# Kernel optimization log

Hardware: AMD Instinct MI355X
Metric: run time of the kernel (lower is better)

## Reference

```python
import jax, jax.numpy as jnp
import numpy as np

N_NODES = 50000
N_EDGES = 600000
IN_DIM = 128
OUT_DIM = 128
N_REL = 32
N_BASES = 4
BN_EPS = 1e-5


def setup_inputs() -> dict:
    key = jax.random.key(0)
    ks = jax.random.split(key, 8)
    entity_emb = jax.random.normal(ks[0], (N_NODES, IN_DIM), dtype=jnp.float32)
    bases = jax.random.normal(ks[1], (N_BASES, IN_DIM, OUT_DIM), dtype=jnp.float32) * 0.05
    coefficients = jax.random.normal(ks[2], (N_REL, N_BASES), dtype=jnp.float32) * 0.5
    W_loop = jax.random.normal(ks[3], (IN_DIM, OUT_DIM), dtype=jnp.float32) * 0.05
    b_loop = jnp.zeros((OUT_DIM,), dtype=jnp.float32)
    gamma = jnp.ones((OUT_DIM,), dtype=jnp.float32)
    beta = jnp.zeros((OUT_DIM,), dtype=jnp.float32)
    edge_index = jax.random.randint(ks[4], (2, N_EDGES), 0, N_NODES, dtype=jnp.int32)
    edge_type = jax.random.randint(ks[5], (N_EDGES,), 0, N_REL, dtype=jnp.int32)
    return {"entity_emb": entity_emb, "bases": bases, "coefficients": coefficients,
            "W_loop": W_loop, "b_loop": b_loop, "gamma": gamma, "beta": beta,
            "edge_index": edge_index, "edge_type": edge_type}


def reference(entity_emb, bases, coefficients, W_loop, b_loop, gamma, beta, edge_index, edge_type):
    N = entity_emb.shape[0]
    # self-loop linear
    out = entity_emb @ W_loop + b_loop  # [N, out_dim]
    # basis decomposition: per-relation weight W[r] = sum_b coeff[r,b] * bases[b]
    W = jnp.einsum('rb,bio->rio', coefficients, bases)  # [R, in, out]
    src, dst = edge_index[0], edge_index[1]
    # per-edge message: entity_emb[src_e] @ W[edge_type_e]  (vectorizes the per-relation loop)
    msg = jnp.einsum('ei,eio->eo', entity_emb[src], W[edge_type])  # [E, out]
    out = out + jax.ops.segment_sum(msg, dst, num_segments=N)
    # degree normalization (in-degree over all edges, clamped at 1)
    deg = jax.ops.segment_sum(jnp.ones_like(dst, dtype=out.dtype), dst, num_segments=N)
    out = out / jnp.maximum(deg, 1.0)[:, None]
    # BatchNorm1d (training mode: biased batch stats over node dim)
    mean = jnp.mean(out, axis=0)
    var = jnp.mean((out - mean) ** 2, axis=0)
    out = (out - mean) / jnp.sqrt(var + BN_EPS) * gamma + beta
    return jax.nn.relu(out)
```

## Files before the change

kernel.cpp:

```cpp
#include <hip/hip_runtime.h>
#include <cstdint>

#define NN 50000
#define NE 600000

typedef unsigned short ushort_t;
typedef __bf16 bf16_t;
typedef __attribute__((ext_vector_type(8))) bf16_t bf16x8;
typedef __attribute__((ext_vector_type(8))) ushort_t ushort8;
typedef __attribute__((ext_vector_type(4))) float f32x4;

#define G_OFF    0ul
#define XBF_OFF  12800000ul
#define CNT_OFF  16000000ul
#define CUR_OFF  16050000ul
#define BSUM_OFF 16100000ul
#define BSCN_OFF 16100128ul
#define CS_OFF   16100256ul
#define CSQ_OFF  16100384ul
#define WT_OFF   16100512ul

__device__ __forceinline__ float2 bf2_to_f2(uint32_t u) {
    float2 r;
    r.x = __uint_as_float(u << 16);
    r.y = __uint_as_float(u & 0xffff0000u);
    return r;
}

__device__ __forceinline__ ushort_t f2bf(float f) {
    uint32_t u = __float_as_uint(f);
    u = (u + 0x7fffu + ((u >> 16) & 1u)) >> 16;
    return (ushort_t)u;
}

__device__ __forceinline__ uint32_t f2bf2(float x, float y) {
    return (uint32_t)f2bf(x) | ((uint32_t)f2bf(y) << 16);
}

__device__ __forceinline__ int swz(int g, int r) {
    return (g & 0x78) | ((g ^ r) & 7);
}

__global__ __launch_bounds__(256) void k_prep(
    const float* __restrict__ Wl, const float* __restrict__ bases,
    ushort_t* __restrict__ WT)
{
    const int i = blockIdx.x * 256 + threadIdx.x;
    if (i >= 128 * 640) return;
    const int n = i / 640;
    const int kk = i - n * 640;
    float v;
    if (kk < 128) v = Wl[kk * 128 + n];
    else {
        const int j = kk - 128;
        v = bases[(size_t)(j >> 7) * 16384 + (j & 127) * 128 + n];
    }
    WT[i] = f2bf(v);
}

__global__ __launch_bounds__(256) void k_cast(
    const float* __restrict__ X, ushort_t* __restrict__ Xbf)
{
    const int i = blockIdx.x * 256 + threadIdx.x;
    if (i >= NN * 16) return;
    const float4* p = (const float4*)(X + (size_t)i * 8);
    const float4 a = p[0], b = p[1];
    ushort_t t8[8] = { f2bf(a.x), f2bf(a.y), f2bf(a.z), f2bf(a.w),
                       f2bf(b.x), f2bf(b.y), f2bf(b.z), f2bf(b.w) };
    *(uint4*)(Xbf + (size_t)i * 8) = *(const uint4*)t8;
}

__global__ __launch_bounds__(256) void k_hist(
    const int* __restrict__ eidx, int* __restrict__ cnt)
{
    const int* __restrict__ dst = eidx + NE;
    for (int e = blockIdx.x * 256 + threadIdx.x; e < NE; e += gridDim.x * 256)
        atomicAdd(cnt + dst[e], 1);
}

__global__ __launch_bounds__(256) void k_scan1(
    const int* __restrict__ cnt, int* __restrict__ curs, int* __restrict__ bsum)
{
    __shared__ int sh[256];
    const int tid = threadIdx.x;
    const int i0 = blockIdx.x * 512 + tid * 2;
    const int v0 = (i0 < NN) ? cnt[i0] : 0;
    const int v1 = (i0 + 1 < NN) ? cnt[i0 + 1] : 0;
    int s = v0 + v1;
    sh[tid] = s;
    __syncthreads();
#pragma unroll
    for (int off = 1; off < 256; off <<= 1) {
        int t = (tid >= off) ? sh[tid - off] : 0;
        __syncthreads();
        sh[tid] += t;
        __syncthreads();
    }
    const int excl = sh[tid] - s;
    if (i0 < NN) curs[i0] = excl;
    if (i0 + 1 < NN) curs[i0 + 1] = excl + v0;
    if (tid == 255) bsum[blockIdx.x] = sh[255];
}

__global__ __launch_bounds__(128) void k_scan2(
    const int* __restrict__ bsum, int* __restrict__ bscan, int nblk)
{
    __shared__ int sh[128];
    const int tid = threadIdx.x;
    int v = (tid < nblk) ? bsum[tid] : 0;
    sh[tid] = v;
    __syncthreads();
#pragma unroll
    for (int off = 1; off < 128; off <<= 1) {
        int t = (tid >= off) ? sh[tid - off] : 0;
        __syncthreads();
        sh[tid] += t;
        __syncthreads();
    }
    if (tid < nblk) bscan[tid] = sh[tid] - v;
}

__global__ __launch_bounds__(256) void k_scan3(
    int* __restrict__ curs, const int* __restrict__ bscan)
{
    const int add = bscan[blockIdx.x];
    const int i0 = blockIdx.x * 512 + threadIdx.x * 2;
    if (i0 < NN) curs[i0] += add;
    if (i0 + 1 < NN) curs[i0 + 1] += add;
}

__global__ __launch_bounds__(256) void k_scatter(
    const int* __restrict__ eidx, const int* __restrict__ etype,
    int* __restrict__ curs, uint32_t* __restrict__ epack)
{
    const int* __restrict__ src = eidx;
    const int* __restrict__ dst = eidx + NE;
    for (int e = blockIdx.x * 256 + threadIdx.x; e < NE; e += gridDim.x * 256) {
        const int d = dst[e];
        const int pos = atomicAdd(curs + d, 1);
        epack[pos] = (uint32_t)src[e] | ((uint32_t)etype[e] << 16);
    }
}

__device__ __forceinline__ void edge_accum(
    uint32_t ep, const ushort_t* __restrict__ Xbf,
    const float* __restrict__ coeff, int lane,
    float2& m0, float2& m1, float2& m2, float2& m3)
{
    const int s = ep & 0xffff;
    const int t = ep >> 16;
    const float4 cw = *(const float4*)(coeff + t * 4);
    const uint32_t xv = *(const uint32_t*)(Xbf + (size_t)s * 128 + lane * 2);
    const float2 x = bf2_to_f2(xv);
    m0.x += cw.x * x.x; m0.y += cw.x * x.y;
    m1.x += cw.y * x.x; m1.y += cw.y * x.y;
    m2.x += cw.z * x.x; m2.y += cw.z * x.y;
    m3.x += cw.w * x.x; m3.y += cw.w * x.y;
}

__global__ __launch_bounds__(256) void k_gather(
    const ushort_t* __restrict__ Xbf, const uint32_t* __restrict__ epack,
    const int* __restrict__ cnt, const int* __restrict__ curs,
    const float* __restrict__ coeff, ushort_t* __restrict__ G)
{
    const int lane = threadIdx.x & 63;
    const int d = (blockIdx.x * 256 + threadIdx.x) >> 6;
    if (d >= NN) return;

    const int n = cnt[d];
    const int end = curs[d];
    int j = end - n;

    float2 m0 = {0.f, 0.f}, m1 = {0.f, 0.f}, m2 = {0.f, 0.f}, m3 = {0.f, 0.f};
    for (; j + 3 < end; j += 4) {
        const uint32_t e0 = epack[j];
        const uint32_t e1 = epack[j + 1];
        const uint32_t e2 = epack[j + 2];
        const uint32_t e3 = epack[j + 3];
        edge_accum(e0, Xbf, coeff, lane, m0, m1, m2, m3);
        edge_accum(e1, Xbf, coeff, lane, m0, m1, m2, m3);
        edge_accum(e2, Xbf, coeff, lane, m0, m1, m2, m3);
        edge_accum(e3, Xbf, coeff, lane, m0, m1, m2, m3);
    }
    for (; j < end; ++j) edge_accum(epack[j], Xbf, coeff, lane, m0, m1, m2, m3);

    uint32_t* gp = (uint32_t*)(G + (size_t)d * 512) + lane;
    gp[0]   = f2bf2(m0.x, m0.y);
    gp[64]  = f2bf2(m1.x, m1.y);
    gp[128] = f2bf2(m2.x, m2.y);
    gp[192] = f2bf2(m3.x, m3.y);
}

__global__ __launch_bounds__(256) void k_gemm_f(
    const ushort_t* __restrict__ Xbf, const ushort_t* __restrict__ G,
    const ushort_t* __restrict__ WT, const float* __restrict__ bl,
    const int* __restrict__ cnt, float* __restrict__ out,
    float* __restrict__ colsum, float* __restrict__ colsq)
{
    __shared__ ushort_t As[32][648];
    const int tid = threadIdx.x;
    const int row0 = blockIdx.x * 32;

    {
        const int r = tid >> 3;
        const int t = tid & 7;
        const int srow = row0 + r;
        const ushort_t* xs = Xbf + (size_t)srow * 128 + t * 8;
        const ushort_t* gs = G   + (size_t)srow * 512 + t * 8;
#pragma unroll
        for (int c = 0; c < 2; ++c) {
            const uint4 v = *(const uint4*)(xs + c * 64);
            *(uint4*)&As[r][swz(c * 8 + t, r) * 8] = v;
        }
#pragma unroll
        for (int c = 2; c < 10; ++c) {
            const uint4 v = *(const uint4*)(gs + (c - 2) * 64);
            *(uint4*)&As[r][swz(c * 8 + t, r) * 8] = v;
        }
    }
    __syncthreads();

    const int lane = tid & 63;
    const int w = tid >> 6;
    const int m = lane & 15;
    const int quad = lane >> 4;

    const ushort_t* bp0 = WT + (size_t)(w * 32 + m) * 640 + quad * 8;
    const ushort_t* bp1 = bp0 + 16 * 640;

    f32x4 cc[2][2];
#pragma unroll
    for (int rt = 0; rt < 2; ++rt)
#pragma unroll
        for (int ct = 0; ct < 2; ++ct)
#pragma unroll
            for (int i = 0; i < 4; ++i) cc[rt][ct][i] = 0.f;

#pragma unroll
    for (int chunk = 0; chunk < 20; ++chunk) {
        const bf16x8 b0 = __builtin_bit_cast(bf16x8,
            *(const ushort8*)(bp0 + chunk * 32));
        const bf16x8 b1 = __builtin_bit_cast(bf16x8,
            *(const ushort8*)(bp1 + chunk * 32));
        const int goff = swz(chunk * 4 + quad, m) * 8;
        const bf16x8 a0 = __builtin_bit_cast(bf16x8,
            *(const ushort8*)&As[m][goff]);
        const bf16x8 a1 = __builtin_bit_cast(bf16x8,
            *(const ushort8*)&As[16 + m][goff]);
        cc[0][0] = __builtin_amdgcn_mfma_f32_16x16x32_bf16(a0, b0, cc[0][0], 0, 0, 0);
        cc[0][1] = __builtin_amdgcn_mfma_f32_16x16x32_bf16(a0, b1, cc[0][1], 0, 0, 0);
        cc[1][0] = __builtin_amdgcn_mfma_f32_16x16x32_bf16(a1, b0, cc[1][0], 0, 0, 0);
        cc[1][1] = __builtin_amdgcn_mfma_f32_16x16x32_bf16(a1, b1, cc[1][1], 0, 0, 0);
    }

    const float blv0 = bl[w * 32 + m];
    const float blv1 = bl[w * 32 + 16 + m];
    float s0 = 0.f, q0 = 0.f, s1 = 0.f, q1 = 0.f;

#pragma unroll
    for (int rt = 0; rt < 2; ++rt) {
        const int rowb = row0 + rt * 16 + quad * 4;
#pragma unroll
        for (int r = 0; r < 4; ++r) {
            const int row = rowb + r;
            if (row < NN) {
                const int dg = cnt[row];
                const float inv = 1.0f / (float)((dg > 0) ? dg : 1);
                float* po = out + (size_t)row * 128 + w * 32 + m;
                const float v0 = (cc[rt][0][r] + blv0) * inv;
                const float v1 = (cc[rt][1][r] + blv1) * inv;
                po[0]  = v0;
                po[16] = v1;
                s0 += v0; q0 += v0 * v0;
                s1 += v1; q1 += v1 * v1;
            }
        }
    }

    s0 += __shfl_down(s0, 32); q0 += __shfl_down(q0, 32);
    s0 += __shfl_down(s0, 16); q0 += __shfl_down(q0, 16);
    s1 += __shfl_down(s1, 32); q1 += __shfl_down(q1, 32);
    s1 += __shfl_down(s1, 16); q1 += __shfl_down(q1, 16);
    if (lane < 16) {
        atomicAdd(colsum + w * 32 + lane, s0);
        atomicAdd(colsq  + w * 32 + lane, q0);
        atomicAdd(colsum + w * 32 + 16 + lane, s1);
        atomicAdd(colsq  + w * 32 + 16 + lane, q1);
    }
}

__global__ __launch_bounds__(256) void k_bn_relu(
    float* __restrict__ out, const float* __restrict__ colsum,
    const float* __restrict__ colsq, const float* __restrict__ gamma,
    const float* __restrict__ beta)
{
    __shared__ float sc[128], sh[128];
    const int tid = threadIdx.x;
    if (tid < 128) {
        const float mean = colsum[tid] * (1.0f / NN);
        const float var = colsq[tid] * (1.0f / NN) - mean * mean;
        const float g = gamma[tid] * rsqrtf(var + 1e-5f);
        sc[tid] = g;
        sh[tid] = beta[tid] - mean * g;
    }
    __syncthreads();
    const int total = NN * 32;
    for (int i = blockIdx.x * 256 + tid; i < total; i += gridDim.x * 256) {
        const int c = (i & 31) << 2;
        float4 v = *(float4*)(out + (size_t)i * 4);
        v.x = fmaxf(fmaf(v.x, sc[c + 0], sh[c + 0]), 0.f);
        v.y = fmaxf(fmaf(v.y, sc[c + 1], sh[c + 1]), 0.f);
        v.z = fmaxf(fmaf(v.z, sc[c + 2], sh[c + 2]), 0.f);
        v.w = fmaxf(fmaf(v.w, sc[c + 3], sh[c + 3]), 0.f);
        *(float4*)(out + (size_t)i * 4) = v;
    }
}

extern "C" void kernel_launch(void* const* d_in, const int* in_sizes, int n_in,
                              void* d_out, int out_size, void* d_ws, size_t ws_size,
                              hipStream_t stream)
{
    const float* X      = (const float*)d_in[0];
    const float* bases  = (const float*)d_in[1];
    const float* coeff  = (const float*)d_in[2];
    const float* Wl     = (const float*)d_in[3];
    const float* bl     = (const float*)d_in[4];
    const float* gamma  = (const float*)d_in[5];
    const float* beta   = (const float*)d_in[6];
    const int*   eidx   = (const int*)d_in[7];
    const int*   etype  = (const int*)d_in[8];
    float* out = (float*)d_out;

    float* ws = (float*)d_ws;
    ushort_t* G      = (ushort_t*)(ws + G_OFF);
    ushort_t* Xbf    = (ushort_t*)(ws + XBF_OFF);
    int*      cnt    = (int*)(ws + CNT_OFF);
    int*      curs   = (int*)(ws + CUR_OFF);
    int*      bsum   = (int*)(ws + BSUM_OFF);
    int*      bscan  = (int*)(ws + BSCN_OFF);
    float*    colsum = ws + CS_OFF;
    float*    colsq  = ws + CSQ_OFF;
    ushort_t* WT     = (ushort_t*)(ws + WT_OFF);
    uint32_t* epack  = (uint32_t*)d_out;

    hipMemsetAsync(cnt, 0, (CSQ_OFF + 128 - CNT_OFF) * sizeof(float), stream);

    const int nblk_scan = (NN + 511) / 512;

    k_prep<<<(128 * 640 + 255) / 256, 256, 0, stream>>>(Wl, bases, WT);
    k_cast<<<(NN * 16 + 255) / 256, 256, 0, stream>>>(X, Xbf);
    k_hist<<<512, 256, 0, stream>>>(eidx, cnt);
    k_scan1<<<nblk_scan, 256, 0, stream>>>(cnt, curs, bsum);
    k_scan2<<<1, 128, 0, stream>>>(bsum, bscan, nblk_scan);
    k_scan3<<<nblk_scan, 256, 0, stream>>>(curs, bscan);
    k_scatter<<<512, 256, 0, stream>>>(eidx, etype, curs, epack);
    k_gather<<<(NN + 3) / 4, 256, 0, stream>>>(Xbf, epack, cnt, curs, coeff, G);
    k_gemm_f<<<(NN + 31) / 32, 256, 0, stream>>>(
        Xbf, G, WT, bl, cnt, out, colsum, colsq);
    k_bn_relu<<<1024, 256, 0, stream>>>(out, colsum, colsq, gamma, beta);
}
```

Before: 292.1 us.

## Store GEMM A-operand in MFMA-tiled layout and load it with async global-to-LDS copies

The cast and gather kernels now write the bf16 node features and the basis-aggregated messages into one tile-blocked buffer (16 nodes × 640 K per tile), already ordered the way the MFMA fragment loads expect. The GEMM kernel can then fill shared memory with contiguous `global_load_lds` 16-byte copies instead of swizzled per-thread stores. The aim is to cut staging and bank-conflict overhead in the GEMM prologue. In exchange, each gather wave now handles four destination nodes one after another, which cuts the number of waves in flight for the latency-bound gather. The transposing cast also adds an extra LDS pass.

Result: slower. 306.0 us (+4.8%).

```diff
diff --git a/kernel.cpp b/kernel.cpp
--- a/kernel.cpp
+++ b/kernel.cpp
@@ -10,15 +10,15 @@
 typedef __attribute__((ext_vector_type(8))) ushort_t ushort8;
 typedef __attribute__((ext_vector_type(4))) float f32x4;
 
-#define G_OFF    0ul
-#define XBF_OFF  12800000ul
-#define CNT_OFF  16000000ul
-#define CUR_OFF  16050000ul
-#define BSUM_OFF 16100000ul
-#define BSCN_OFF 16100128ul
-#define CS_OFF   16100256ul
-#define CSQ_OFF  16100384ul
-#define WT_OFF   16100512ul
+#define WT_OFF   0ul
+#define XG_OFF   40960ul
+#define XBF_OFF  16040960ul
+#define CNT_OFF  19240960ul
+#define CUR_OFF  19290960ul
+#define BSUM_OFF 19340960ul
+#define BSCN_OFF 19341088ul
+#define CS_OFF   19341216ul
+#define CSQ_OFF  19341344ul
 
 __device__ __forceinline__ float2 bf2_to_f2(uint32_t u) {
     float2 r;
@@ -37,8 +37,10 @@
     return (uint32_t)f2bf(x) | ((uint32_t)f2bf(y) << 16);
 }
 
-__device__ __forceinline__ int swz(int g, int r) {
-    return (g & 0x78) | ((g ^ r) & 7);
+__device__ __forceinline__ void async_copy16(const void* g, void* l) {
+    __builtin_amdgcn_global_load_lds(
+        (const __attribute__((address_space(1))) void*)g,
+        (__attribute__((address_space(3))) void*)l, 16, 0, 0);
 }
 
 __global__ __launch_bounds__(256) void k_prep(
@@ -59,15 +61,29 @@
 }
 
 __global__ __launch_bounds__(256) void k_cast(
-    const float* __restrict__ X, ushort_t* __restrict__ Xbf)
-{
-    const int i = blockIdx.x * 256 + threadIdx.x;
-    if (i >= NN * 16) return;
-    const float4* p = (const float4*)(X + (size_t)i * 8);
-    const float4 a = p[0], b = p[1];
-    ushort_t t8[8] = { f2bf(a.x), f2bf(a.y), f2bf(a.z), f2bf(a.w),
-                       f2bf(b.x), f2bf(b.y), f2bf(b.z), f2bf(b.w) };
-    *(uint4*)(Xbf + (size_t)i * 8) = *(const uint4*)t8;
+    const float* __restrict__ X, ushort_t* __restrict__ Xbf,
+    ushort_t* __restrict__ XG)
+{
+    __shared__ ushort_t L[16][136];
+    const int tid = threadIdx.x;
+    const int tile = blockIdx.x;
+    {
+        const int row = tid >> 4, gc = tid & 15;
+        const int node = tile * 16 + row;
+        const float4* p = (const float4*)(X + (size_t)node * 128 + gc * 8);
+        const float4 a = p[0], b = p[1];
+        ushort_t t8[8] = { f2bf(a.x), f2bf(a.y), f2bf(a.z), f2bf(a.w),
+                           f2bf(b.x), f2bf(b.y), f2bf(b.z), f2bf(b.w) };
+        const uint4 v = *(const uint4*)t8;
+        *(uint4*)&L[row][gc * 8] = v;
+        *(uint4*)(Xbf + (size_t)node * 128 + gc * 8) = v;
+    }
+    __syncthreads();
+    {
+        const int g = tid >> 4, r2 = tid & 15;
+        const uint4 u = *(const uint4*)&L[r2][g * 8];
+        *(uint4*)(XG + (size_t)tile * 10240 + g * 128 + r2 * 8) = u;
+    }
 }
 
 __global__ __launch_bounds__(256) void k_hist(
@@ -161,70 +177,66 @@
 __global__ __launch_bounds__(256) void k_gather(
     const ushort_t* __restrict__ Xbf, const uint32_t* __restrict__ epack,
     const int* __restrict__ cnt, const int* __restrict__ curs,
-    const float* __restrict__ coeff, ushort_t* __restrict__ G)
+    const float* __restrict__ coeff, ushort_t* __restrict__ XG)
 {
     const int lane = threadIdx.x & 63;
-    const int d = (blockIdx.x * 256 + threadIdx.x) >> 6;
-    if (d >= NN) return;
-
-    const int n = cnt[d];
-    const int end = curs[d];
-    int j = end - n;
-
-    float2 m0 = {0.f, 0.f}, m1 = {0.f, 0.f}, m2 = {0.f, 0.f}, m3 = {0.f, 0.f};
-    for (; j + 3 < end; j += 4) {
-        const uint32_t e0 = epack[j];
-        const uint32_t e1 = epack[j + 1];
-        const uint32_t e2 = epack[j + 2];
-        const uint32_t e3 = epack[j + 3];
-        edge_accum(e0, Xbf, coeff, lane, m0, m1, m2, m3);
-        edge_accum(e1, Xbf, coeff, lane, m0, m1, m2, m3);
-        edge_accum(e2, Xbf, coeff, lane, m0, m1, m2, m3);
-        edge_accum(e3, Xbf, coeff, lane, m0, m1, m2, m3);
-    }
-    for (; j < end; ++j) edge_accum(epack[j], Xbf, coeff, lane, m0, m1, m2, m3);
-
-    uint32_t* gp = (uint32_t*)(G + (size_t)d * 512) + lane;
-    gp[0]   = f2bf2(m0.x, m0.y);
-    gp[64]  = f2bf2(m1.x, m1.y);
-    gp[128] = f2bf2(m2.x, m2.y);
-    gp[192] = f2bf2(m3.x, m3.y);
+    const int w = threadIdx.x >> 6;
+    const int tile = blockIdx.x;
+    uint32_t* __restrict__ gbase = (uint32_t*)(XG + (size_t)tile * 10240);
+    const int wbase = (16 + (lane >> 2)) * 64 + (lane & 3);
+
+    for (int i = 0; i < 4; ++i) {
+        const int d = tile * 16 + w * 4 + i;
+        const int n = cnt[d];
+        const int end = curs[d];
+        int j = end - n;
+
+        float2 m0 = {0.f, 0.f}, m1 = {0.f, 0.f}, m2 = {0.f, 0.f}, m3 = {0.f, 0.f};
+        for (; j + 3 < end; j += 4) {
+            const uint32_t e0 = epack[j];
+            const uint32_t e1 = epack[j + 1];
+            const uint32_t e2 = epack[j + 2];
+            const uint32_t e3 = epack[j + 3];
+            edge_accum(e0, Xbf, coeff, lane, m0, m1, m2, m3);
+            edge_accum(e1, Xbf, coeff, lane, m0, m1, m2, m3);
+            edge_accum(e2, Xbf, coeff, lane, m0, m1, m2, m3);
+            edge_accum(e3, Xbf, coeff, lane, m0, m1, m2, m3);
+        }
+        for (; j < end; ++j) edge_accum(epack[j], Xbf, coeff, lane, m0, m1, m2, m3);
+
+        const int word = wbase + (d & 15) * 4;
+        gbase[word]        = f2bf2(m0.x, m0.y);
+        gbase[word + 1024] = f2bf2(m1.x, m1.y);
+        gbase[word + 2048] = f2bf2(m2.x, m2.y);
+        gbase[word + 3072] = f2bf2(m3.x, m3.y);
+    }
 }
 
 __global__ __launch_bounds__(256) void k_gemm_f(
-    const ushort_t* __restrict__ Xbf, const ushort_t* __restrict__ G,
-    const ushort_t* __restrict__ WT, const float* __restrict__ bl,
-    const int* __restrict__ cnt, float* __restrict__ out,
-    float* __restrict__ colsum, float* __restrict__ colsq)
-{
-    __shared__ ushort_t As[32][648];
-    const int tid = threadIdx.x;
-    const int row0 = blockIdx.x * 32;
-
-    {
-        const int r = tid >> 3;
-        const int t = tid & 7;
-        const int srow = row0 + r;
-        const ushort_t* xs = Xbf + (size_t)srow * 128 + t * 8;
-        const ushort_t* gs = G   + (size_t)srow * 512 + t * 8;
-#pragma unroll
-        for (int c = 0; c < 2; ++c) {
-            const uint4 v = *(const uint4*)(xs + c * 64);
-            *(uint4*)&As[r][swz(c * 8 + t, r) * 8] = v;
-        }
-#pragma unroll
-        for (int c = 2; c < 10; ++c) {
-            const uint4 v = *(const uint4*)(gs + (c - 2) * 64);
-            *(uint4*)&As[r][swz(c * 8 + t, r) * 8] = v;
-        }
-    }
-    __syncthreads();
-
+    const ushort_t* __restrict__ XG, const ushort_t* __restrict__ WT,
+    const float* __restrict__ bl, const int* __restrict__ cnt,
+    float* __restrict__ out, float* __restrict__ colsum,
+    float* __restrict__ colsq)
+{
+    __shared__ ushort_t As[2][10240];
+    const int tid = threadIdx.x;
     const int lane = tid & 63;
     const int w = tid >> 6;
+    const int row0 = blockIdx.x * 32;
+    const int tile0 = blockIdx.x * 2;
+
+#pragma unroll
+    for (int k = 0; k < 10; ++k) {
+        const int s = w * 10 + k;
+        const int tl = s >= 20 ? 1 : 0;
+        const int off = s - tl * 20;
+        const ushort_t* src = XG + (size_t)(tile0 + tl) * 10240 + off * 512 + lane * 8;
+        async_copy16(src, &As[tl][off * 512]);
+    }
+    __syncthreads();
+
     const int m = lane & 15;
     const int quad = lane >> 4;
-
     const ushort_t* bp0 = WT + (size_t)(w * 32 + m) * 640 + quad * 8;
     const ushort_t* bp1 = bp0 + 16 * 640;
 
@@ -237,16 +249,12 @@
             for (int i = 0; i < 4; ++i) cc[rt][ct][i] = 0.f;
 
 #pragma unroll
-    for (int chunk = 0; chunk < 20; ++chunk) {
-        const bf16x8 b0 = __builtin_bit_cast(bf16x8,
-            *(const ushort8*)(bp0 + chunk * 32));
-        const bf16x8 b1 = __builtin_bit_cast(bf16x8,
-            *(const ushort8*)(bp1 + chunk * 32));
-        const int goff = swz(chunk * 4 + quad, m) * 8;
-        const bf16x8 a0 = __builtin_bit_cast(bf16x8,
-            *(const ushort8*)&As[m][goff]);
-        const bf16x8 a1 = __builtin_bit_cast(bf16x8,
-            *(const ushort8*)&As[16 + m][goff]);
+    for (int c = 0; c < 20; ++c) {
+        const bf16x8 b0 = __builtin_bit_cast(bf16x8, *(const ushort8*)(bp0 + c * 32));
+        const bf16x8 b1 = __builtin_bit_cast(bf16x8, *(const ushort8*)(bp1 + c * 32));
+        const int aoff = (c * 4 + quad) * 128 + m * 8;
+        const bf16x8 a0 = __builtin_bit_cast(bf16x8, *(const ushort8*)&As[0][aoff]);
+        const bf16x8 a1 = __builtin_bit_cast(bf16x8, *(const ushort8*)&As[1][aoff]);
         cc[0][0] = __builtin_amdgcn_mfma_f32_16x16x32_bf16(a0, b0, cc[0][0], 0, 0, 0);
         cc[0][1] = __builtin_amdgcn_mfma_f32_16x16x32_bf16(a0, b1, cc[0][1], 0, 0, 0);
         cc[1][0] = __builtin_amdgcn_mfma_f32_16x16x32_bf16(a1, b0, cc[1][0], 0, 0, 0);
@@ -332,7 +340,8 @@
     float* out = (float*)d_out;
 
     float* ws = (float*)d_ws;
-    ushort_t* G      = (ushort_t*)(ws + G_OFF);
+    ushort_t* WT     = (ushort_t*)(ws + WT_OFF);
+    ushort_t* XG     = (ushort_t*)(ws + XG_OFF);
     ushort_t* Xbf    = (ushort_t*)(ws + XBF_OFF);
     int*      cnt    = (int*)(ws + CNT_OFF);
     int*      curs   = (int*)(ws + CUR_OFF);
@@ -340,7 +349,6 @@
     int*      bscan  = (int*)(ws + BSCN_OFF);
     float*    colsum = ws + CS_OFF;
     float*    colsq  = ws + CSQ_OFF;
-    ushort_t* WT     = (ushort_t*)(ws + WT_OFF);
     uint32_t* epack  = (uint32_t*)d_out;
 
     hipMemsetAsync(cnt, 0, (CSQ_OFF + 128 - CNT_OFF) * sizeof(float), stream);
@@ -348,14 +356,13 @@
     const int nblk_scan = (NN + 511) / 512;
 
     k_prep<<<(128 * 640 + 255) / 256, 256, 0, stream>>>(Wl, bases, WT);
-    k_cast<<<(NN * 16 + 255) / 256, 256, 0, stream>>>(X, Xbf);
+    k_cast<<<3125, 256, 0, stream>>>(X, Xbf, XG);
     k_hist<<<512, 256, 0, stream>>>(eidx, cnt);
     k_scan1<<<nblk_scan, 256, 0, stream>>>(cnt, curs, bsum);
     k_scan2<<<1, 128, 0, stream>>>(bsum, bscan, nblk_scan);
     k_scan3<<<nblk_scan, 256, 0, stream>>>(curs, bscan);
     k_scatter<<<512, 256, 0, stream>>>(eidx, etype, curs, epack);
-    k_gather<<<(NN + 3) / 4, 256, 0, stream>>>(Xbf, epack, cnt, curs, coeff, G);
-    k_gemm_f<<<(NN + 31) / 32, 256, 0, stream>>>(
-        Xbf, G, WT, bl, cnt, out, colsum, colsq);
+    k_gather<<<3125, 256, 0, stream>>>(Xbf, epack, cnt, curs, coeff, XG);
+    k_gemm_f<<<1563, 256, 0, stream>>>(XG, WT, bl, cnt, out, colsum, colsq);
     k_bn_relu<<<1024, 256, 0, stream>>>(out, colsum, colsq, gamma, beta);
 }
```
